# Kernel tuning notes

Hardware: AMD Instinct MI355X
Metric: run time of the kernel (lower is better)

The kernel has to match this reference:

```python
import jax, jax.numpy as jnp
import numpy as np

B, N, DIM, H, DH = 2, 1024, 1024, 8, 64
DI = H * DH  # 512
K = 4        # depthwise conv kernel
EPS = 1.1920929e-07  # float32 eps (torch RMSNorm default)


def setup_inputs() -> dict:
    key = jax.random.key(0)
    ks = jax.random.split(key, 12)
    s = lambda k, shape, sc=0.02: jax.random.normal(k, shape, jnp.float32) * sc
    return dict(
        x=jax.random.normal(ks[0], (B, N, DIM), jnp.float32),
        w_rms=jnp.ones((DIM,), jnp.float32),
        wq=s(ks[1], (DIM, DI)), wk=s(ks[2], (DIM, DI)), wv=s(ks[3], (DIM, DI)),
        wo=s(ks[4], (DI, DIM)),
        conv_q=s(ks[5], (DIM, K), 0.3), conv_k=s(ks[6], (DIM, K), 0.3), conv_v=s(ks[7], (DIM, K), 0.3),
        gamma_q=jnp.ones((H, 1, DH), jnp.float32), gamma_k=jnp.ones((H, 1, DH), jnp.float32),
        lr_w=s(ks[8], (DIM, H)), lr_b=jnp.full((H,), -4.0, jnp.float32),
        decay_w=s(ks[9], (DIM, H)), decay_b=jnp.full((H,), 4.0, jnp.float32),
        mom_w=s(ks[10], (DIM, H)), mom_b=jnp.full((H,), 2.0, jnp.float32),
    )


def rmsnorm(x, w):
    return x * jax.lax.rsqrt(jnp.mean(x * x, -1, keepdims=True) + EPS) * w


def mh_rmsnorm(x, gamma):  # x: (b, h, n, d)
    rms = jnp.sqrt(jnp.sum(x * x, -1, keepdims=True)) * (DH ** -0.5)
    return x / jnp.maximum(rms, 1e-8) * gamma


def dwconv(x, w):  # x: (b, n, dim), w: (dim, K) depthwise, padding K//2 -> length n+1
    y = jax.lax.conv_general_dilated(
        x.transpose(0, 2, 1), w[:, None, :], (1,), [(K // 2, K // 2)],
        feature_group_count=DIM, dimension_numbers=('NCW', 'OIW', 'NCW'))
    return y.transpose(0, 2, 1)


def gated_scan(a, x):  # h_t = a_t h_{t-1} + x_t, h_{-1}=0; a:(bh,t), x:(bh,t,d,d)
    def combine(c1, c2):
        a1, x1 = c1
        a2, x2 = c2
        return a1 * a2, a2 * x1 + x2
    _, h = jax.lax.associative_scan(combine, (a[..., None, None], x), axis=1)
    return h


def reference(x, w_rms, wq, wk, wv, wo, conv_q, conv_k, conv_v,
              gamma_q, gamma_k, lr_w, lr_b, decay_w, decay_b, mom_w, mom_b):
    b, n, _ = x.shape
    xa = rmsnorm(x, w_rms)
    qi, ki, vi = dwconv(xa, conv_q), dwconv(xa, conv_k), dwconv(xa, conv_v)
    split = lambda t: t.reshape(b, -1, H, DH).transpose(0, 2, 1, 3)[:, :, :n]  # (b,h,n,d)
    q = mh_rmsnorm(split(qi @ wq), gamma_q)
    k = mh_rmsnorm(split(ki @ wk), gamma_k)
    v = split(vi @ wv)
    fq = q.reshape(b * H, n, DH)
    fk = k.reshape(b * H, n, DH)
    fv = v.reshape(b * H, n, DH)
    sig = jax.nn.sigmoid
    lr = sig(xa @ lr_w + lr_b).transpose(0, 2, 1).reshape(b * H, n)
    decay = sig(xa @ decay_w + decay_b).transpose(0, 2, 1).reshape(b * H, n)
    mom = sig(xa @ mom_w + mom_b).transpose(0, 2, 1).reshape(b * H, n)
    # S_ref = S0 = 0 (fresh state) => pred = 0, delta_vec = -v
    g = jnp.einsum('bti,btj->btij', -fv, fk)          # (bh, n, d, d)
    Z = gated_scan(mom, g)                             # momentum scan
    S = gated_scan(decay, -lr[..., None, None] * Z)    # memory scan
    S_prev = jnp.concatenate([jnp.zeros_like(S[:, :1]), S[:, :-1]], axis=1)
    y = jnp.einsum('btdp,btp->btd', S_prev, fq)        # retrieval y_t = S_{t-1} psi_t
    y = y.reshape(b, H, n, DH).transpose(0, 2, 1, 3).reshape(b, n, DI)
    return y @ wo
```

## Files before the change

kernel.cpp:

```cpp
#include <hip/hip_runtime.h>
#include <math.h>

#define DEV __device__ __forceinline__

constexpr int Bb   = 2;
constexpr int Seq  = 1024;
constexpr int Dim  = 1024;
constexpr int Hh   = 8;
constexpr int Dh   = 64;
constexpr int Di   = 512;
constexpr int BN   = Bb * Seq;
constexpr int NSEQ = Bb * Hh;
constexpr int CHUNK = 32;
constexpr int CLEN  = Seq / CHUNK;
constexpr float EPSV = 1.1920929e-07f;
constexpr int NT   = 16;

typedef _Float16 half8 __attribute__((ext_vector_type(8)));
typedef float    f32x4 __attribute__((ext_vector_type(4)));

DEV float bf2f(unsigned short u) {
  union { unsigned int i; float f; } x; x.i = ((unsigned int)u) << 16; return x.f;
}
DEV unsigned short f2bf(float f) {
  union { float f; unsigned int i; } x; x.f = f;
  unsigned int r = x.i + 0x7fffu + ((x.i >> 16) & 1u);
  return (unsigned short)(r >> 16);
}
DEV float ldin(const void* p, int f32, size_t i) {
  if (f32) return ((const float*)p)[i];
  return bf2f(((const unsigned short*)p)[i]);
}

struct InPtrs { const void* p[17]; int n[17]; };

__global__ __launch_bounds__(64) void k_sniff(InPtrs ip, int* __restrict__ flags) {
  int b = blockIdx.x, tid = threadIdx.x;
  const unsigned short* u = (const unsigned short*)ip.p[b];
  int count = ip.n[b];
  int j = 2 * tid;
  int valid = 0, bad = 0;
  if (j < count) {
    valid = 1;
    float v = bf2f(u[j]);
    float a = fabsf(v);
    if (!(a >= 1e-12f && a <= 1e4f)) bad = 1;
  }
#pragma unroll
  for (int m = 1; m < 64; m <<= 1) { valid += __shfl_xor(valid, m); bad += __shfl_xor(bad, m); }
  if (tid == 0) flags[b] = (2 * bad > valid) ? 1 : 0;
}

__global__ __launch_bounds__(256) void k_prep_all(
    const void* __restrict__ wq, const void* __restrict__ wk,
    const void* __restrict__ wv, const void* __restrict__ wo,
    const void* __restrict__ lr_w, const void* __restrict__ decay_w,
    const void* __restrict__ mom_w,
    const void* __restrict__ cq, const void* __restrict__ ck,
    const void* __restrict__ cv,
    const void* __restrict__ gq, const void* __restrict__ gk,
    const void* __restrict__ lr_b, const void* __restrict__ decay_b,
    const void* __restrict__ mom_b,
    const int* __restrict__ flags,
    _Float16* __restrict__ wqT, _Float16* __restrict__ wkT,
    _Float16* __restrict__ wvT, _Float16* __restrict__ woT,
    _Float16* __restrict__ WgT,
    _Float16* __restrict__ wcq, _Float16* __restrict__ wck,
    _Float16* __restrict__ wcv,
    float* __restrict__ gqf, float* __restrict__ gkf, float* __restrict__ gbf)
{
  int blk = blockIdx.x;
  int tid = threadIdx.x;

  if (blk < 1024) {
    int z = blk >> 8, bx = blk & 15, by = (blk >> 4) & 15;
    const void* src = (z == 0) ? wq : ((z == 1) ? wk : ((z == 2) ? wv : wo));
    _Float16* dst   = (z == 0) ? wqT : ((z == 1) ? wkT : ((z == 2) ? wvT : woT));
    int f = flags[(z == 0) ? 2 : ((z == 1) ? 3 : ((z == 2) ? 4 : 5))];
    int Kd = (z < 3) ? Dim : Di;
    int Nn = (z < 3) ? Di : Dim;
    int n0 = bx * 64, k0 = by * 64;
    if (n0 >= Nn || k0 >= Kd) return;

    __shared__ float tile[64][65];
    int r = tid >> 4, c4 = (tid & 15) * 4;
#pragma unroll
    for (int rr = 0; rr < 4; ++rr) {
      int k = rr * 16 + r;
#pragma unroll
      for (int j = 0; j < 4; ++j)
        tile[k][c4 + j] = ldin(src, f, (size_t)(k0 + k) * Nn + n0 + c4 + j);
    }
    __syncthreads();
#pragma unroll
    for (int rr = 0; rr < 4; ++rr) {
      int n = rr * 16 + r;
      _Float16 o4[4];
#pragma unroll
      for (int j = 0; j < 4; ++j) o4[j] = (_Float16)tile[c4 + j][n];
      *(ushort4*)&dst[(size_t)(n0 + n) * Kd + k0 + c4] = *(ushort4*)o4;
    }
  } else if (blk < 1088) {
    int row = blk - 1024;
    if (row < 24) {
      int g = row >> 3, h = row & 7;
      const void* W = (g == 0) ? lr_w : ((g == 1) ? decay_w : mom_w);
      int f = (g == 0) ? flags[11] : ((g == 1) ? flags[13] : flags[15]);
#pragma unroll
      for (int it = 0; it < 4; ++it) {
        int d = it * 256 + tid;
        WgT[(size_t)row * Dim + d] = (_Float16)ldin(W, f, (size_t)d * Hh + h);
      }
    } else {
#pragma unroll
      for (int it = 0; it < 4; ++it)
        WgT[(size_t)row * Dim + it * 256 + tid] = (_Float16)0.f;
    }
  } else if (blk < 1104) {
    int e = (blk - 1088) * 256 + tid;
    int f6 = flags[6], f7 = flags[7], f8 = flags[8];
    wcq[e] = (_Float16)ldin(cq, f6, e);
    wck[e] = (_Float16)ldin(ck, f7, e);
    wcv[e] = (_Float16)ldin(cv, f8, e);
  } else {
    int f9 = flags[9], f10 = flags[10];
    for (int i = tid; i < Di; i += 256) {
      gqf[i] = ldin(gq, f9, i);
      gkf[i] = ldin(gk, f10, i);
    }
    if (tid < 24) {
      int g = tid >> 3, h = tid & 7;
      const void* Bp = (g == 0) ? lr_b : ((g == 1) ? decay_b : mom_b);
      int fB = (g == 0) ? flags[12] : ((g == 1) ? flags[14] : flags[16]);
      gbf[tid] = ldin(Bp, fB, h);
    }
  }
}

__global__ __launch_bounds__(256) void k_rms(
    const void* __restrict__ x, const void* __restrict__ w_rms,
    const int* __restrict__ flags, _Float16* __restrict__ xaf)
{
  __shared__ float red[4];
  int r = blockIdx.x;
  int tid = threadIdx.x, lane = tid & 63, wid = tid >> 6;
  int fx = flags[0], fw = flags[1];

  size_t rb = (size_t)r * Dim + tid * 4;
  float v0, v1, v2, v3;
  if (fx) {
    float4 u = *(const float4*)((const float*)x + rb);
    v0 = u.x; v1 = u.y; v2 = u.z; v3 = u.w;
  } else {
    ushort4 u = *(const ushort4*)((const unsigned short*)x + rb);
    v0 = bf2f(u.x); v1 = bf2f(u.y); v2 = bf2f(u.z); v3 = bf2f(u.w);
  }
  float ss = v0 * v0 + v1 * v1 + v2 * v2 + v3 * v3;
#pragma unroll
  for (int m = 1; m < 64; m <<= 1) ss += __shfl_xor(ss, m);
  if (lane == 0) red[wid] = ss;
  __syncthreads();
  float scale = rsqrtf((red[0] + red[1] + red[2] + red[3]) * (1.0f / Dim) + EPSV);

  float w0, w1, w2, w3;
  if (fw) {
    float4 u = *(const float4*)((const float*)w_rms + tid * 4);
    w0 = u.x; w1 = u.y; w2 = u.z; w3 = u.w;
  } else {
    ushort4 u = *(const ushort4*)((const unsigned short*)w_rms + tid * 4);
    w0 = bf2f(u.x); w1 = bf2f(u.y); w2 = bf2f(u.z); w3 = bf2f(u.w);
  }
  _Float16 t4[4] = {(_Float16)(v0 * scale * w0), (_Float16)(v1 * scale * w1),
                    (_Float16)(v2 * scale * w2), (_Float16)(v3 * scale * w3)};
  *(ushort4*)&xaf[rb] = *(ushort4*)t4;
}

__global__ __launch_bounds__(256) void k_gates(
    const _Float16* __restrict__ xaf, const _Float16* __restrict__ WgT,
    const float* __restrict__ gbf,
    float* __restrict__ lr, float* __restrict__ decay, float* __restrict__ mom)
{
  __shared__ __align__(16) _Float16 As[64][40];
  __shared__ __align__(16) _Float16 Bs[64][40];

  int tid = threadIdx.x, lane = tid & 63, wvid = tid >> 6;
  int m0 = blockIdx.x * 64;
  int srow = tid >> 2, scol = (tid & 3) * 8;
  int mrow = lane & 15, quad = lane >> 4;

  f32x4 acc[4];
#pragma unroll
  for (int mi = 0; mi < 4; ++mi) acc[mi] = (f32x4){0.f, 0.f, 0.f, 0.f};

  for (int kt = 0; kt < Dim; kt += 32) {
    __syncthreads();
    *(uint4*)&As[srow][scol] = *(const uint4*)&xaf[(size_t)(m0 + srow) * Dim + kt + scol];
    *(uint4*)&Bs[srow][scol] = *(const uint4*)&WgT[(size_t)srow * Dim + kt + scol];
    __syncthreads();
    half8 bfr = *(const half8*)&Bs[wvid * 16 + mrow][quad * 8];
#pragma unroll
    for (int mi = 0; mi < 4; ++mi) {
      half8 afr = *(const half8*)&As[mi * 16 + mrow][quad * 8];
      acc[mi] = __builtin_amdgcn_mfma_f32_16x16x32_f16(afr, bfr, acc[mi], 0, 0, 0);
    }
  }

  int col = wvid * 16 + mrow;
  if (col < 24) {
    int g = col >> 3, h = col & 7;
    float bias = gbf[col];
    float* Op = (g == 0) ? lr : ((g == 1) ? decay : mom);
#pragma unroll
    for (int mi = 0; mi < 4; ++mi) {
#pragma unroll
      for (int r2 = 0; r2 < 4; ++r2) {
        int row = m0 + mi * 16 + quad * 4 + r2;
        int b = row >> 10, t = row & (Seq - 1);
        float z = acc[mi][r2] + bias;
        Op[(b * Hh + h) * Seq + t] = 1.f / (1.f + expf(-z));
      }
    }
  }
}

__global__ __launch_bounds__(256) void k_conv(
    const _Float16* __restrict__ xaf,
    const _Float16* __restrict__ wcq, const _Float16* __restrict__ wck,
    const _Float16* __restrict__ wcv,
    _Float16* __restrict__ qc, _Float16* __restrict__ kc,
    _Float16* __restrict__ vc)
{
  int tb = blockIdx.x, b = blockIdx.y;
  int t0 = tb * NT;
  int c0 = threadIdx.x * 4;

  _Float16 lwq[16], lwk[16], lwv[16];
  *(uint4*)&lwq[0] = *(const uint4*)&wcq[c0 * 4];
  *(uint4*)&lwq[8] = *(const uint4*)&wcq[c0 * 4 + 8];
  *(uint4*)&lwk[0] = *(const uint4*)&wck[c0 * 4];
  *(uint4*)&lwk[8] = *(const uint4*)&wck[c0 * 4 + 8];
  *(uint4*)&lwv[0] = *(const uint4*)&wcv[c0 * 4];
  *(uint4*)&lwv[8] = *(const uint4*)&wcv[c0 * 4 + 8];

  float win[4][4];
  auto loadrow = [&](int ts, float dst[4]) {
    if (ts >= 0 && ts < Seq) {
      ushort4 u = *(const ushort4*)&xaf[((size_t)(b * Seq + ts)) * Dim + c0];
      _Float16 hx[4]; *(ushort4*)hx = u;
      dst[0] = (float)hx[0]; dst[1] = (float)hx[1];
      dst[2] = (float)hx[2]; dst[3] = (float)hx[3];
    } else {
      dst[0] = 0.f; dst[1] = 0.f; dst[2] = 0.f; dst[3] = 0.f;
    }
  };
  loadrow(t0 - 2, win[0]);
  loadrow(t0 - 1, win[1]);
  loadrow(t0,     win[2]);

#pragma unroll
  for (int tt = 0; tt < NT; ++tt) {
    int t = t0 + tt;
    loadrow(t + 1, win[(tt + 3) & 3]);
    const float* r0 = win[(tt + 0) & 3];
    const float* r1 = win[(tt + 1) & 3];
    const float* r2 = win[(tt + 2) & 3];
    const float* r3 = win[(tt + 3) & 3];

    _Float16 tq[4], tk[4], tv[4];
#pragma unroll
    for (int j = 0; j < 4; ++j) {
      float aq = r0[j] * (float)lwq[j * 4 + 0] + r1[j] * (float)lwq[j * 4 + 1]
               + r2[j] * (float)lwq[j * 4 + 2] + r3[j] * (float)lwq[j * 4 + 3];
      float ak = r0[j] * (float)lwk[j * 4 + 0] + r1[j] * (float)lwk[j * 4 + 1]
               + r2[j] * (float)lwk[j * 4 + 2] + r3[j] * (float)lwk[j * 4 + 3];
      float av = r0[j] * (float)lwv[j * 4 + 0] + r1[j] * (float)lwv[j * 4 + 1]
               + r2[j] * (float)lwv[j * 4 + 2] + r3[j] * (float)lwv[j * 4 + 3];
      tq[j] = (_Float16)aq; tk[j] = (_Float16)ak; tv[j] = (_Float16)av;
    }
    size_t o = ((size_t)(b * Seq + t)) * Dim + c0;
    *(ushort4*)&qc[o] = *(ushort4*)tq;
    *(ushort4*)&kc[o] = *(ushort4*)tk;
    *(ushort4*)&vc[o] = *(ushort4*)tv;
  }
}

__global__ __launch_bounds__(256) void k_gemm_128(
    const _Float16* __restrict__ A0, const _Float16* __restrict__ A1,
    const _Float16* __restrict__ A2,
    const _Float16* __restrict__ B0, const _Float16* __restrict__ B1,
    const _Float16* __restrict__ B2,
    void* __restrict__ C0, void* __restrict__ C1, void* __restrict__ C2,
    const int* __restrict__ flags,
    int Nn, int Kd, int is_final)
{
  int z = blockIdx.z;
  const _Float16* A  = (z == 0) ? A0 : ((z == 1) ? A1 : A2);
  const _Float16* Bt = (z == 0) ? B0 : ((z == 1) ? B1 : B2);
  void* C = (z == 0) ? C0 : ((z == 1) ? C1 : C2);

  __shared__ __align__(16) _Float16 As[128][40];
  __shared__ __align__(16) _Float16 Bs[64][40];

  int tid = threadIdx.x, lane = tid & 63, wv = tid >> 6;
  int n0 = blockIdx.x * 64, m0 = blockIdx.y * 128;
  int mrow = lane & 15, quad = lane >> 4;
  int wm = wv * 32;

  int ar0 = tid >> 2,        ac0 = (tid & 3) * 8;
  int ar1 = (tid + 256) >> 2;

  f32x4 acc[2][4];
#pragma unroll
  for (int mi = 0; mi < 2; ++mi)
#pragma unroll
    for (int ni = 0; ni < 4; ++ni) acc[mi][ni] = (f32x4){0.f, 0.f, 0.f, 0.f};

  for (int kt = 0; kt < Kd; kt += 32) {
    __syncthreads();
    *(uint4*)&As[ar0][ac0] = *(const uint4*)&A[(size_t)(m0 + ar0) * Kd + kt + ac0];
    *(uint4*)&As[ar1][ac0] = *(const uint4*)&A[(size_t)(m0 + ar1) * Kd + kt + ac0];
    *(uint4*)&Bs[ar0][ac0] = *(const uint4*)&Bt[(size_t)(n0 + ar0) * Kd + kt + ac0];
    __syncthreads();

    half8 bfr[4];
#pragma unroll
    for (int ni = 0; ni < 4; ++ni)
      bfr[ni] = *(const half8*)&Bs[ni * 16 + mrow][quad * 8];
#pragma unroll
    for (int mi = 0; mi < 2; ++mi) {
      half8 afr = *(const half8*)&As[wm + mi * 16 + mrow][quad * 8];
#pragma unroll
      for (int ni = 0; ni < 4; ++ni)
        acc[mi][ni] = __builtin_amdgcn_mfma_f32_16x16x32_f16(afr, bfr[ni], acc[mi][ni], 0, 0, 0);
    }
  }

  int any_bf16 = 0;
  if (is_final) {
#pragma unroll
    for (int i2 = 0; i2 < 17; ++i2) any_bf16 |= (flags[i2] == 0);
  }

#pragma unroll
  for (int mi = 0; mi < 2; ++mi) {
#pragma unroll
    for (int ni = 0; ni < 4; ++ni) {
      int col = n0 + ni * 16 + mrow;
#pragma unroll
      for (int r2 = 0; r2 < 4; ++r2) {
        int row = m0 + wm + mi * 16 + quad * 4 + r2;
        float v = acc[mi][ni][r2];
        size_t idx = (size_t)row * Nn + col;
        if (!is_final)        ((_Float16*)C)[idx] = (_Float16)v;
        else if (any_bf16)    ((unsigned short*)C)[idx] = f2bf(v);
        else                  ((float*)C)[idx] = v;
      }
    }
  }
}

__global__ __launch_bounds__(256) void k_phaseA(
    const _Float16* __restrict__ kpre, const _Float16* __restrict__ vpre,
    const float* __restrict__ gkf,
    const float* __restrict__ lr, const float* __restrict__ decay,
    const float* __restrict__ mom,
    _Float16* __restrict__ ZS_Z, _Float16* __restrict__ ZS_S,
    float* __restrict__ Mc, float* __restrict__ Dc, float* __restrict__ Wc)
{
  int c = blockIdx.x, s = blockIdx.y;
  int b = s >> 3, h = s & 7;
  int tid = threadIdx.x, lane = tid & 63, wv = tid >> 6;
  int i = tid >> 2, j0 = (tid & 3) * 16;
  __shared__ float kn[CLEN][64], vv[CLEN][64];
  __shared__ float gl[CLEN], gd[CLEN], gm[CLEN];

  {
    int t = tid >> 3, col = (tid & 7) * 8;
    size_t g = ((size_t)(b * Seq + c * CLEN + t)) * Di + h * 64 + col;
    half8 kv = *(const half8*)&kpre[g];
    half8 vvv = *(const half8*)&vpre[g];
#pragma unroll
    for (int j = 0; j < 8; ++j) { kn[t][col + j] = (float)kv[j]; vv[t][col + j] = (float)vvv[j]; }
    if (tid < 96) {
      int which = tid >> 5, t2 = tid & 31;
      const float* gp = (which == 0) ? lr : ((which == 1) ? decay : mom);
      float val = gp[s * Seq + c * CLEN + t2];
      if (which == 0) gl[t2] = val; else if (which == 1) gd[t2] = val; else gm[t2] = val;
    }
  }
  __syncthreads();
  {
    float gk = gkf[h * 64 + lane];
#pragma unroll
    for (int tt = 0; tt < 8; ++tt) {
      int t = wv * 8 + tt;
      float kvv = kn[t][lane];
      float ss = kvv * kvv;
#pragma unroll
      for (int m = 1; m < 64; m <<= 1) ss += __shfl_xor(ss, m);
      kn[t][lane] = kvv * (1.f / fmaxf(sqrtf(ss) * 0.125f, 1e-8f)) * gk;
    }
  }
  __syncthreads();

  float Zl[16], Sl[16];
#pragma unroll
  for (int jj = 0; jj < 16; ++jj) { Zl[jj] = 0.f; Sl[jj] = 0.f; }
  float Mcum = 1.f, Dcum = 1.f, wacc = 0.f;

  for (int t = 0; t < CLEN; ++t) {
    float l = gl[t], dd = gd[t], mm = gm[t];
    float vi = vv[t][i];
    Mcum *= mm;
#pragma unroll
    for (int jj = 0; jj < 16; ++jj) {
      Zl[jj] = fmaf(mm, Zl[jj], -vi * kn[t][j0 + jj]);
      Sl[jj] = fmaf(dd, Sl[jj], -l * Zl[jj]);
    }
    wacc = fmaf(dd, wacc, -l * Mcum);
    Dcum *= dd;
  }
  size_t base = ((size_t)(s * CHUNK + c)) * 4096 + (size_t)i * 64 + j0;
  half8 zo0, zo1, so0, so1;
#pragma unroll
  for (int jj = 0; jj < 8; ++jj) {
    zo0[jj] = (_Float16)Zl[jj];     zo1[jj] = (_Float16)Zl[jj + 8];
    so0[jj] = (_Float16)Sl[jj];     so1[jj] = (_Float16)Sl[jj + 8];
  }
  *(half8*)&ZS_Z[base] = zo0; *(half8*)&ZS_Z[base + 8] = zo1;
  *(half8*)&ZS_S[base] = so0; *(half8*)&ZS_S[base + 8] = so1;
  if (tid == 0) {
    Mc[s * CHUNK + c] = Mcum; Dc[s * CHUNK + c] = Dcum; Wc[s * CHUNK + c] = wacc;
  }
}

__global__ __launch_bounds__(256) void k_phaseB(
    _Float16* __restrict__ ZS_Z, _Float16* __restrict__ ZS_S,
    const float* __restrict__ Mc, const float* __restrict__ Dc,
    const float* __restrict__ Wc)
{
  int s = blockIdx.x;
  int e = blockIdx.y * 256 + threadIdx.x;
  float Z = 0.f, S = 0.f;
  for (int c = 0; c < CHUNK; ++c) {
    size_t base = ((size_t)(s * CHUNK + c)) * 4096 + e;
    float mc = Mc[s * CHUNK + c], dc = Dc[s * CHUNK + c], wc = Wc[s * CHUNK + c];
    float zl = (float)ZS_Z[base], sl = (float)ZS_S[base];
    ZS_Z[base] = (_Float16)Z; ZS_S[base] = (_Float16)S;
    S = fmaf(dc, S, fmaf(wc, Z, sl));
    Z = fmaf(mc, Z, zl);
  }
}

__global__ __launch_bounds__(256) void k_phaseC(
    const _Float16* __restrict__ qpre, const _Float16* __restrict__ kpre,
    const _Float16* __restrict__ vpre,
    const float* __restrict__ gqf, const float* __restrict__ gkf,
    const float* __restrict__ lr, const float* __restrict__ decay,
    const float* __restrict__ mom,
    const _Float16* __restrict__ ZS_Z, const _Float16* __restrict__ ZS_S,
    _Float16* __restrict__ yb)
{
  int c = blockIdx.x, s = blockIdx.y;
  int b = s >> 3, h = s & 7;
  int tid = threadIdx.x, lane = tid & 63, wv = tid >> 6;
  int i = tid >> 2, j0 = (tid & 3) * 16;
  __shared__ float kn[CLEN][64], vv[CLEN][64], qn[CLEN][64];
  __shared__ float gl[CLEN], gd[CLEN], gm[CLEN];

  float Zi_[16], Si_[16], Zl[16], Sl[16];
  size_t base = ((size_t)(s * CHUNK + c)) * 4096 + (size_t)i * 64 + j0;
  {
    half8 z0 = *(const half8*)&ZS_Z[base], z1 = *(const half8*)&ZS_Z[base + 8];
    half8 s0 = *(const half8*)&ZS_S[base], s1 = *(const half8*)&ZS_S[base + 8];
#pragma unroll
    for (int jj = 0; jj < 8; ++jj) {
      Zi_[jj] = (float)z0[jj]; Zi_[jj + 8] = (float)z1[jj];
      Si_[jj] = (float)s0[jj]; Si_[jj + 8] = (float)s1[jj];
      Zl[jj] = 0.f; Zl[jj + 8] = 0.f; Sl[jj] = 0.f; Sl[jj + 8] = 0.f;
    }
  }
  {
    int t = tid >> 3, col = (tid & 7) * 8;
    size_t g = ((size_t)(b * Seq + c * CLEN + t)) * Di + h * 64 + col;
    half8 kv = *(const half8*)&kpre[g];
    half8 vvv = *(const half8*)&vpre[g];
    half8 qv = *(const half8*)&qpre[g];
#pragma unroll
    for (int j = 0; j < 8; ++j) {
      kn[t][col + j] = (float)kv[j]; vv[t][col + j] = (float)vvv[j];
      qn[t][col + j] = (float)qv[j];
    }
    if (tid < 96) {
      int which = tid >> 5, t2 = tid & 31;
      const float* gp = (which == 0) ? lr : ((which == 1) ? decay : mom);
      float val = gp[s * Seq + c * CLEN + t2];
      if (which == 0) gl[t2] = val; else if (which == 1) gd[t2] = val; else gm[t2] = val;
    }
  }
  __syncthreads();
  {
    float gk = gkf[h * 64 + lane];
    float gq = gqf[h * 64 + lane];
#pragma unroll
    for (int tt = 0; tt < 8; ++tt) {
      int t = wv * 8 + tt;
      float kvv = kn[t][lane];
      float ssk = kvv * kvv;
      float qvv = qn[t][lane];
      float ssq = qvv * qvv;
#pragma unroll
      for (int m = 1; m < 64; m <<= 1) { ssk += __shfl_xor(ssk, m); ssq += __shfl_xor(ssq, m); }
      kn[t][lane] = kvv * (1.f / fmaxf(sqrtf(ssk) * 0.125f, 1e-8f)) * gk;
      qn[t][lane] = qvv * (1.f / fmaxf(sqrtf(ssq) * 0.125f, 1e-8f)) * gq;
    }
  }
  __syncthreads();

  float Mcum = 1.f, Dcum = 1.f, wacc = 0.f;
  float Dprev = 1.f, wprev = 0.f;

  for (int t = 0; t < CLEN; ++t) {
    float l = gl[t], dd = gd[t], mm = gm[t];

    float yp = 0.f;
#pragma unroll
    for (int jj = 0; jj < 16; ++jj) {
      float tmp = fmaf(Dprev, Si_[jj], fmaf(wprev, Zi_[jj], Sl[jj]));
      yp = fmaf(tmp, qn[t][j0 + jj], yp);
    }
    yp += __shfl_xor(yp, 1);
    yp += __shfl_xor(yp, 2);
    if ((tid & 3) == 0)
      yb[((size_t)(b * Seq + c * CLEN + t)) * Di + h * 64 + i] = (_Float16)yp;

    float vi = vv[t][i];
    Mcum *= mm;
#pragma unroll
    for (int jj = 0; jj < 16; ++jj) {
      Zl[jj] = fmaf(mm, Zl[jj], -vi * kn[t][j0 + jj]);
      Sl[jj] = fmaf(dd, Sl[jj], -l * Zl[jj]);
    }
    wacc = fmaf(dd, wacc, -l * Mcum);
    Dcum *= dd;
    Dprev = Dcum; wprev = wacc;
  }
}

extern "C" void kernel_launch(void* const* d_in, const int* in_sizes, int n_in,
                              void* d_out, int out_size, void* d_ws, size_t ws_size,
                              hipStream_t stream) {
  InPtrs ip;
  for (int i = 0; i < 17; ++i) { ip.p[i] = d_in[i]; ip.n[i] = in_sizes[i]; }

  char* p = (char*)d_ws;
  auto take = [&](size_t bytes) -> char* {
    char* q = p; p += (bytes + 255) & ~(size_t)255; return q;
  };
  int* flags           = (int*)take(32 * 4);
  _Float16* xaf        = (_Float16*)take((size_t)BN * Dim * 2);
  _Float16* qc         = (_Float16*)take((size_t)BN * Dim * 2);
  _Float16* kc         = (_Float16*)take((size_t)BN * Dim * 2);
  _Float16* vc         = (_Float16*)take((size_t)BN * Dim * 2);
  _Float16* qpre       = (_Float16*)take((size_t)BN * Di * 2);
  _Float16* kpre       = (_Float16*)take((size_t)BN * Di * 2);
  _Float16* vpre       = (_Float16*)take((size_t)BN * Di * 2);
  float* lrA           = (float*)take((size_t)NSEQ * Seq * 4);
  float* decayA        = (float*)take((size_t)NSEQ * Seq * 4);
  float* momA          = (float*)take((size_t)NSEQ * Seq * 4);
  float* Mc            = (float*)take((size_t)NSEQ * CHUNK * 4);
  float* Dc            = (float*)take((size_t)NSEQ * CHUNK * 4);
  float* Wc            = (float*)take((size_t)NSEQ * CHUNK * 4);
  _Float16* wqT        = (_Float16*)take((size_t)Di * Dim * 2);
  _Float16* wkT        = (_Float16*)take((size_t)Di * Dim * 2);
  _Float16* wvT        = (_Float16*)take((size_t)Di * Dim * 2);
  _Float16* woT        = (_Float16*)take((size_t)Dim * Di * 2);
  _Float16* WgT        = (_Float16*)take((size_t)64 * Dim * 2);
  _Float16* wcq        = (_Float16*)take((size_t)Dim * 4 * 2);
  _Float16* wck        = (_Float16*)take((size_t)Dim * 4 * 2);
  _Float16* wcv        = (_Float16*)take((size_t)Dim * 4 * 2);
  float* gqf           = (float*)take(Di * 4);
  float* gkf           = (float*)take(Di * 4);
  float* gbf           = (float*)take(32 * 4);
  _Float16* ZS_Z       = qc;
  _Float16* ZS_S       = kc;
  _Float16* yb         = vc;

  k_sniff<<<17, 64, 0, stream>>>(ip, flags);
  k_prep_all<<<1105, 256, 0, stream>>>(
      d_in[2], d_in[3], d_in[4], d_in[5],
      d_in[11], d_in[13], d_in[15],
      d_in[6], d_in[7], d_in[8],
      d_in[9], d_in[10], d_in[12], d_in[14], d_in[16],
      flags, wqT, wkT, wvT, woT, WgT, wcq, wck, wcv, gqf, gkf, gbf);

  k_rms<<<BN, 256, 0, stream>>>(d_in[0], d_in[1], flags, xaf);
  k_gates<<<BN / 64, 256, 0, stream>>>(xaf, WgT, gbf, lrA, decayA, momA);
  k_conv<<<dim3(Seq / NT, Bb), 256, 0, stream>>>(xaf, wcq, wck, wcv, qc, kc, vc);

  dim3 g1(Di / 64, BN / 128, 3);
  k_gemm_128<<<g1, 256, 0, stream>>>(qc, kc, vc, wqT, wkT, wvT,
                                     qpre, kpre, vpre, flags, Di, Dim, 0);

  k_phaseA<<<dim3(CHUNK, NSEQ), 256, 0, stream>>>(kpre, vpre, gkf,
                                                  lrA, decayA, momA,
                                                  ZS_Z, ZS_S, Mc, Dc, Wc);
  k_phaseB<<<dim3(NSEQ, 16), 256, 0, stream>>>(ZS_Z, ZS_S, Mc, Dc, Wc);
  k_phaseC<<<dim3(CHUNK, NSEQ), 256, 0, stream>>>(qpre, kpre, vpre, gqf, gkf,
                                                  lrA, decayA, momA,
                                                  ZS_Z, ZS_S, yb);

  dim3 g2(Dim / 64, BN / 128, 1);
  k_gemm_128<<<g2, 256, 0, stream>>>(yb, yb, yb, woT, woT, woT,
                                     d_out, d_out, d_out, flags, Dim, Di, 1);
}
```

Baseline: 208.4 us.

## Fuse RMSNorm with depthwise conv, split-K gate GEMM, fold sniff into prep

Merges the dtype-sniff kernel into the weight-prep kernel, so each prep block recomputes its own input format flag. Fuses RMSNorm into the depthwise conv kernel, normalizing rows with halo into shared memory and writing xaf once. Splits the gate GEMM over K into eight partial slabs, and moves the reduction, bias and sigmoid into the scan phase kernels. The aim is fewer launches and more parallelism in the small gate GEMM, at the cost of redundant halo normalization, redundant sniffing per prep block, and extra partial-sum reads in phaseA and phaseC.

Result: faster. 195.6 us (-6.1%).

```diff
diff --git a/kernel.cpp b/kernel.cpp
--- a/kernel.cpp
+++ b/kernel.cpp
@@ -14,7 +14,8 @@
 constexpr int CHUNK = 32;
 constexpr int CLEN  = Seq / CHUNK;
 constexpr float EPSV = 1.1920929e-07f;
-constexpr int NT   = 16;
+constexpr int NT2  = 8;
+constexpr int KSPL = 8;
 
 typedef _Float16 half8 __attribute__((ext_vector_type(8)));
 typedef float    f32x4 __attribute__((ext_vector_type(4)));
@@ -31,37 +32,24 @@
   if (f32) return ((const float*)p)[i];
   return bf2f(((const unsigned short*)p)[i]);
 }
-
-struct InPtrs { const void* p[17]; int n[17]; };
-
-__global__ __launch_bounds__(64) void k_sniff(InPtrs ip, int* __restrict__ flags) {
-  int b = blockIdx.x, tid = threadIdx.x;
-  const unsigned short* u = (const unsigned short*)ip.p[b];
-  int count = ip.n[b];
-  int j = 2 * tid;
-  int valid = 0, bad = 0;
-  if (j < count) {
+DEV int sniff_vote(const void* p, int n, int tid) {
+  int j = 2 * tid, valid = 0, bad = 0;
+  if (j < n) {
     valid = 1;
-    float v = bf2f(u[j]);
+    float v = bf2f(((const unsigned short*)p)[j]);
     float a = fabsf(v);
     if (!(a >= 1e-12f && a <= 1e4f)) bad = 1;
   }
 #pragma unroll
   for (int m = 1; m < 64; m <<= 1) { valid += __shfl_xor(valid, m); bad += __shfl_xor(bad, m); }
-  if (tid == 0) flags[b] = (2 * bad > valid) ? 1 : 0;
-}
+  return (2 * bad > valid) ? 1 : 0;
+}
+
+struct InPtrs { const void* p[17]; int n[17]; };
 
 __global__ __launch_bounds__(256) void k_prep_all(
-    const void* __restrict__ wq, const void* __restrict__ wk,
-    const void* __restrict__ wv, const void* __restrict__ wo,
-    const void* __restrict__ lr_w, const void* __restrict__ decay_w,
-    const void* __restrict__ mom_w,
-    const void* __restrict__ cq, const void* __restrict__ ck,
-    const void* __restrict__ cv,
-    const void* __restrict__ gq, const void* __restrict__ gk,
-    const void* __restrict__ lr_b, const void* __restrict__ decay_b,
-    const void* __restrict__ mom_b,
-    const int* __restrict__ flags,
+    InPtrs ip,
+    int* __restrict__ flags,
     _Float16* __restrict__ wqT, _Float16* __restrict__ wkT,
     _Float16* __restrict__ wvT, _Float16* __restrict__ woT,
     _Float16* __restrict__ WgT,
@@ -71,17 +59,22 @@
 {
   int blk = blockIdx.x;
   int tid = threadIdx.x;
+  __shared__ int sfl[8];
 
   if (blk < 1024) {
     int z = blk >> 8, bx = blk & 15, by = (blk >> 4) & 15;
-    const void* src = (z == 0) ? wq : ((z == 1) ? wk : ((z == 2) ? wv : wo));
+    int idx = (z == 0) ? 2 : ((z == 1) ? 3 : ((z == 2) ? 4 : 5));
+    const void* src = ip.p[idx];
     _Float16* dst   = (z == 0) ? wqT : ((z == 1) ? wkT : ((z == 2) ? wvT : woT));
-    int f = flags[(z == 0) ? 2 : ((z == 1) ? 3 : ((z == 2) ? 4 : 5))];
     int Kd = (z < 3) ? Dim : Di;
     int Nn = (z < 3) ? Di : Dim;
     int n0 = bx * 64, k0 = by * 64;
     if (n0 >= Nn || k0 >= Kd) return;
 
+    if (tid < 64) { int f = sniff_vote(src, ip.n[idx], tid); if (tid == 0) sfl[0] = f; }
+    __syncthreads();
+    int f = sfl[0];
+
     __shared__ float tile[64][65];
     int r = tid >> 4, c4 = (tid & 15) * 4;
 #pragma unroll
@@ -104,8 +97,11 @@
     int row = blk - 1024;
     if (row < 24) {
       int g = row >> 3, h = row & 7;
-      const void* W = (g == 0) ? lr_w : ((g == 1) ? decay_w : mom_w);
-      int f = (g == 0) ? flags[11] : ((g == 1) ? flags[13] : flags[15]);
+      int idx = (g == 0) ? 11 : ((g == 1) ? 13 : 15);
+      const void* W = ip.p[idx];
+      if (tid < 64) { int f = sniff_vote(W, ip.n[idx], tid); if (tid == 0) sfl[0] = f; }
+      __syncthreads();
+      int f = sfl[0];
 #pragma unroll
       for (int it = 0; it < 4; ++it) {
         int d = it * 256 + tid;
@@ -117,122 +113,94 @@
         WgT[(size_t)row * Dim + it * 256 + tid] = (_Float16)0.f;
     }
   } else if (blk < 1104) {
+    if (tid < 64) {
+      int f6 = sniff_vote(ip.p[6], ip.n[6], tid);
+      int f7 = sniff_vote(ip.p[7], ip.n[7], tid);
+      int f8 = sniff_vote(ip.p[8], ip.n[8], tid);
+      if (tid == 0) { sfl[0] = f6; sfl[1] = f7; sfl[2] = f8; }
+    }
+    __syncthreads();
     int e = (blk - 1088) * 256 + tid;
-    int f6 = flags[6], f7 = flags[7], f8 = flags[8];
-    wcq[e] = (_Float16)ldin(cq, f6, e);
-    wck[e] = (_Float16)ldin(ck, f7, e);
-    wcv[e] = (_Float16)ldin(cv, f8, e);
+    wcq[e] = (_Float16)ldin(ip.p[6], sfl[0], e);
+    wck[e] = (_Float16)ldin(ip.p[7], sfl[1], e);
+    wcv[e] = (_Float16)ldin(ip.p[8], sfl[2], e);
   } else {
-    int f9 = flags[9], f10 = flags[10];
+    __shared__ int allf[17];
+    for (int ii = 0; ii < 17; ++ii) {
+      if (tid < 64) {
+        int f = sniff_vote(ip.p[ii], ip.n[ii], tid);
+        if (tid == 0) { flags[ii] = f; allf[ii] = f; }
+      }
+    }
+    __syncthreads();
+    int f9 = allf[9], f10 = allf[10];
     for (int i = tid; i < Di; i += 256) {
-      gqf[i] = ldin(gq, f9, i);
-      gkf[i] = ldin(gk, f10, i);
+      gqf[i] = ldin(ip.p[9], f9, i);
+      gkf[i] = ldin(ip.p[10], f10, i);
     }
     if (tid < 24) {
       int g = tid >> 3, h = tid & 7;
-      const void* Bp = (g == 0) ? lr_b : ((g == 1) ? decay_b : mom_b);
-      int fB = (g == 0) ? flags[12] : ((g == 1) ? flags[14] : flags[16]);
-      gbf[tid] = ldin(Bp, fB, h);
-    }
-  }
-}
-
-__global__ __launch_bounds__(256) void k_rms(
+      int idx = (g == 0) ? 12 : ((g == 1) ? 14 : 16);
+      gbf[tid] = ldin(ip.p[idx], allf[idx], h);
+    }
+  }
+}
+
+__global__ __launch_bounds__(256) void k_rmsconv(
     const void* __restrict__ x, const void* __restrict__ w_rms,
-    const int* __restrict__ flags, _Float16* __restrict__ xaf)
-{
+    const int* __restrict__ flags,
+    const _Float16* __restrict__ wcq, const _Float16* __restrict__ wck,
+    const _Float16* __restrict__ wcv,
+    _Float16* __restrict__ xaf,
+    _Float16* __restrict__ qc, _Float16* __restrict__ kc,
+    _Float16* __restrict__ vc)
+{
+  constexpr int NR = NT2 + 3;
+  __shared__ _Float16 xas[NR][Dim];
   __shared__ float red[4];
-  int r = blockIdx.x;
+  int tb = blockIdx.x, b = blockIdx.y;
+  int t0 = tb * NT2;
   int tid = threadIdx.x, lane = tid & 63, wid = tid >> 6;
+  int c0 = tid * 4;
   int fx = flags[0], fw = flags[1];
-
-  size_t rb = (size_t)r * Dim + tid * 4;
-  float v0, v1, v2, v3;
-  if (fx) {
-    float4 u = *(const float4*)((const float*)x + rb);
-    v0 = u.x; v1 = u.y; v2 = u.z; v3 = u.w;
-  } else {
-    ushort4 u = *(const ushort4*)((const unsigned short*)x + rb);
-    v0 = bf2f(u.x); v1 = bf2f(u.y); v2 = bf2f(u.z); v3 = bf2f(u.w);
-  }
-  float ss = v0 * v0 + v1 * v1 + v2 * v2 + v3 * v3;
-#pragma unroll
-  for (int m = 1; m < 64; m <<= 1) ss += __shfl_xor(ss, m);
-  if (lane == 0) red[wid] = ss;
-  __syncthreads();
-  float scale = rsqrtf((red[0] + red[1] + red[2] + red[3]) * (1.0f / Dim) + EPSV);
 
   float w0, w1, w2, w3;
   if (fw) {
-    float4 u = *(const float4*)((const float*)w_rms + tid * 4);
+    float4 u = *(const float4*)((const float*)w_rms + c0);
     w0 = u.x; w1 = u.y; w2 = u.z; w3 = u.w;
   } else {
-    ushort4 u = *(const ushort4*)((const unsigned short*)w_rms + tid * 4);
+    ushort4 u = *(const ushort4*)((const unsigned short*)w_rms + c0);
     w0 = bf2f(u.x); w1 = bf2f(u.y); w2 = bf2f(u.z); w3 = bf2f(u.w);
   }
-  _Float16 t4[4] = {(_Float16)(v0 * scale * w0), (_Float16)(v1 * scale * w1),
-                    (_Float16)(v2 * scale * w2), (_Float16)(v3 * scale * w3)};
-  *(ushort4*)&xaf[rb] = *(ushort4*)t4;
-}
-
-__global__ __launch_bounds__(256) void k_gates(
-    const _Float16* __restrict__ xaf, const _Float16* __restrict__ WgT,
-    const float* __restrict__ gbf,
-    float* __restrict__ lr, float* __restrict__ decay, float* __restrict__ mom)
-{
-  __shared__ __align__(16) _Float16 As[64][40];
-  __shared__ __align__(16) _Float16 Bs[64][40];
-
-  int tid = threadIdx.x, lane = tid & 63, wvid = tid >> 6;
-  int m0 = blockIdx.x * 64;
-  int srow = tid >> 2, scol = (tid & 3) * 8;
-  int mrow = lane & 15, quad = lane >> 4;
-
-  f32x4 acc[4];
-#pragma unroll
-  for (int mi = 0; mi < 4; ++mi) acc[mi] = (f32x4){0.f, 0.f, 0.f, 0.f};
-
-  for (int kt = 0; kt < Dim; kt += 32) {
-    __syncthreads();
-    *(uint4*)&As[srow][scol] = *(const uint4*)&xaf[(size_t)(m0 + srow) * Dim + kt + scol];
-    *(uint4*)&Bs[srow][scol] = *(const uint4*)&WgT[(size_t)srow * Dim + kt + scol];
-    __syncthreads();
-    half8 bfr = *(const half8*)&Bs[wvid * 16 + mrow][quad * 8];
-#pragma unroll
-    for (int mi = 0; mi < 4; ++mi) {
-      half8 afr = *(const half8*)&As[mi * 16 + mrow][quad * 8];
-      acc[mi] = __builtin_amdgcn_mfma_f32_16x16x32_f16(afr, bfr, acc[mi], 0, 0, 0);
-    }
-  }
-
-  int col = wvid * 16 + mrow;
-  if (col < 24) {
-    int g = col >> 3, h = col & 7;
-    float bias = gbf[col];
-    float* Op = (g == 0) ? lr : ((g == 1) ? decay : mom);
-#pragma unroll
-    for (int mi = 0; mi < 4; ++mi) {
-#pragma unroll
-      for (int r2 = 0; r2 < 4; ++r2) {
-        int row = m0 + mi * 16 + quad * 4 + r2;
-        int b = row >> 10, t = row & (Seq - 1);
-        float z = acc[mi][r2] + bias;
-        Op[(b * Hh + h) * Seq + t] = 1.f / (1.f + expf(-z));
+
+  for (int rr = 0; rr < NR; ++rr) {
+    int r = t0 - 2 + rr;
+    float v0 = 0.f, v1 = 0.f, v2 = 0.f, v3 = 0.f;
+    bool inr = (r >= 0 && r < Seq);
+    if (inr) {
+      size_t rb = (size_t)(b * Seq + r) * Dim + c0;
+      if (fx) {
+        float4 u = *(const float4*)((const float*)x + rb);
+        v0 = u.x; v1 = u.y; v2 = u.z; v3 = u.w;
+      } else {
+        ushort4 u = *(const ushort4*)((const unsigned short*)x + rb);
+        v0 = bf2f(u.x); v1 = bf2f(u.y); v2 = bf2f(u.z); v3 = bf2f(u.w);
       }
     }
-  }
-}
-
-__global__ __launch_bounds__(256) void k_conv(
-    const _Float16* __restrict__ xaf,
-    const _Float16* __restrict__ wcq, const _Float16* __restrict__ wck,
-    const _Float16* __restrict__ wcv,
-    _Float16* __restrict__ qc, _Float16* __restrict__ kc,
-    _Float16* __restrict__ vc)
-{
-  int tb = blockIdx.x, b = blockIdx.y;
-  int t0 = tb * NT;
-  int c0 = threadIdx.x * 4;
+    float ss = v0 * v0 + v1 * v1 + v2 * v2 + v3 * v3;
+#pragma unroll
+    for (int m = 1; m < 64; m <<= 1) ss += __shfl_xor(ss, m);
+    if (lane == 0) red[wid] = ss;
+    __syncthreads();
+    float scale = rsqrtf((red[0] + red[1] + red[2] + red[3]) * (1.0f / Dim) + EPSV);
+
+    _Float16 t4[4] = {(_Float16)(v0 * scale * w0), (_Float16)(v1 * scale * w1),
+                      (_Float16)(v2 * scale * w2), (_Float16)(v3 * scale * w3)};
+    *(ushort4*)&xas[rr][c0] = *(ushort4*)t4;
+    if (inr && r >= t0 && r < t0 + NT2)
+      *(ushort4*)&xaf[(size_t)(b * Seq + r) * Dim + c0] = *(ushort4*)t4;
+    __syncthreads();
+  }
 
   _Float16 lwq[16], lwk[16], lwv[16];
   *(uint4*)&lwq[0] = *(const uint4*)&wcq[c0 * 4];
@@ -242,45 +210,74 @@
   *(uint4*)&lwv[0] = *(const uint4*)&wcv[c0 * 4];
   *(uint4*)&lwv[8] = *(const uint4*)&wcv[c0 * 4 + 8];
 
-  float win[4][4];
-  auto loadrow = [&](int ts, float dst[4]) {
-    if (ts >= 0 && ts < Seq) {
-      ushort4 u = *(const ushort4*)&xaf[((size_t)(b * Seq + ts)) * Dim + c0];
-      _Float16 hx[4]; *(ushort4*)hx = u;
-      dst[0] = (float)hx[0]; dst[1] = (float)hx[1];
-      dst[2] = (float)hx[2]; dst[3] = (float)hx[3];
-    } else {
-      dst[0] = 0.f; dst[1] = 0.f; dst[2] = 0.f; dst[3] = 0.f;
-    }
-  };
-  loadrow(t0 - 2, win[0]);
-  loadrow(t0 - 1, win[1]);
-  loadrow(t0,     win[2]);
-
-#pragma unroll
-  for (int tt = 0; tt < NT; ++tt) {
-    int t = t0 + tt;
-    loadrow(t + 1, win[(tt + 3) & 3]);
-    const float* r0 = win[(tt + 0) & 3];
-    const float* r1 = win[(tt + 1) & 3];
-    const float* r2 = win[(tt + 2) & 3];
-    const float* r3 = win[(tt + 3) & 3];
-
+#pragma unroll
+  for (int tt = 0; tt < NT2; ++tt) {
+    float rv[4][4];
+#pragma unroll
+    for (int k = 0; k < 4; ++k) {
+      _Float16 hx[4];
+      *(ushort4*)hx = *(const ushort4*)&xas[tt + k][c0];
+#pragma unroll
+      for (int j = 0; j < 4; ++j) rv[k][j] = (float)hx[j];
+    }
     _Float16 tq[4], tk[4], tv[4];
 #pragma unroll
     for (int j = 0; j < 4; ++j) {
-      float aq = r0[j] * (float)lwq[j * 4 + 0] + r1[j] * (float)lwq[j * 4 + 1]
-               + r2[j] * (float)lwq[j * 4 + 2] + r3[j] * (float)lwq[j * 4 + 3];
-      float ak = r0[j] * (float)lwk[j * 4 + 0] + r1[j] * (float)lwk[j * 4 + 1]
-               + r2[j] * (float)lwk[j * 4 + 2] + r3[j] * (float)lwk[j * 4 + 3];
-      float av = r0[j] * (float)lwv[j * 4 + 0] + r1[j] * (float)lwv[j * 4 + 1]
-               + r2[j] * (float)lwv[j * 4 + 2] + r3[j] * (float)lwv[j * 4 + 3];
+      float aq = rv[0][j] * (float)lwq[j * 4 + 0] + rv[1][j] * (float)lwq[j * 4 + 1]
+               + rv[2][j] * (float)lwq[j * 4 + 2] + rv[3][j] * (float)lwq[j * 4 + 3];
+      float ak = rv[0][j] * (float)lwk[j * 4 + 0] + rv[1][j] * (float)lwk[j * 4 + 1]
+               + rv[2][j] * (float)lwk[j * 4 + 2] + rv[3][j] * (float)lwk[j * 4 + 3];
+      float av = rv[0][j] * (float)lwv[j * 4 + 0] + rv[1][j] * (float)lwv[j * 4 + 1]
+               + rv[2][j] * (float)lwv[j * 4 + 2] + rv[3][j] * (float)lwv[j * 4 + 3];
       tq[j] = (_Float16)aq; tk[j] = (_Float16)ak; tv[j] = (_Float16)av;
     }
-    size_t o = ((size_t)(b * Seq + t)) * Dim + c0;
+    size_t o = ((size_t)(b * Seq + t0 + tt)) * Dim + c0;
     *(ushort4*)&qc[o] = *(ushort4*)tq;
     *(ushort4*)&kc[o] = *(ushort4*)tk;
     *(ushort4*)&vc[o] = *(ushort4*)tv;
+  }
+}
+
+__global__ __launch_bounds__(256) void k_gates(
+    const _Float16* __restrict__ xaf, const _Float16* __restrict__ WgT,
+    float* __restrict__ gpart)
+{
+  __shared__ __align__(16) _Float16 As[64][40];
+  __shared__ __align__(16) _Float16 Bs[64][40];
+
+  int tid = threadIdx.x, lane = tid & 63, wvid = tid >> 6;
+  int m0 = blockIdx.x * 64, ks = blockIdx.y;
+  int srow = tid >> 2, scol = (tid & 3) * 8;
+  int mrow = lane & 15, quad = lane >> 4;
+  int kbase = ks * (Dim / KSPL);
+
+  f32x4 acc[4];
+#pragma unroll
+  for (int mi = 0; mi < 4; ++mi) acc[mi] = (f32x4){0.f, 0.f, 0.f, 0.f};
+
+  for (int kt = kbase; kt < kbase + Dim / KSPL; kt += 32) {
+    __syncthreads();
+    *(uint4*)&As[srow][scol] = *(const uint4*)&xaf[(size_t)(m0 + srow) * Dim + kt + scol];
+    *(uint4*)&Bs[srow][scol] = *(const uint4*)&WgT[(size_t)srow * Dim + kt + scol];
+    __syncthreads();
+    half8 bfr = *(const half8*)&Bs[wvid * 16 + mrow][quad * 8];
+#pragma unroll
+    for (int mi = 0; mi < 4; ++mi) {
+      half8 afr = *(const half8*)&As[mi * 16 + mrow][quad * 8];
+      acc[mi] = __builtin_amdgcn_mfma_f32_16x16x32_f16(afr, bfr, acc[mi], 0, 0, 0);
+    }
+  }
+
+  int col = wvid * 16 + mrow;
+  if (col < 24) {
+#pragma unroll
+    for (int mi = 0; mi < 4; ++mi) {
+#pragma unroll
+      for (int r2 = 0; r2 < 4; ++r2) {
+        int row = m0 + mi * 16 + quad * 4 + r2;
+        gpart[((size_t)ks * BN + row) * 32 + col] = acc[mi][r2];
+      }
+    }
   }
 }
 
@@ -306,7 +303,7 @@
   int mrow = lane & 15, quad = lane >> 4;
   int wm = wv * 32;
 
-  int ar0 = tid >> 2,        ac0 = (tid & 3) * 8;
+  int ar0 = tid >> 2, ac0 = (tid & 3) * 8;
   int ar1 = (tid + 256) >> 2;
 
   f32x4 acc[2][4];
@@ -359,11 +356,27 @@
   }
 }
 
+DEV void load_gates(const float* __restrict__ gpart, const float* __restrict__ gbf,
+                    int b, int h, int c, int tid,
+                    float* gl, float* gd, float* gm)
+{
+  if (tid < 96) {
+    int which = tid >> 5, t2 = tid & 31;
+    int col = which * 8 + h;
+    int row = b * Seq + c * CLEN + t2;
+    float acc = gbf[col];
+#pragma unroll
+    for (int ks = 0; ks < KSPL; ++ks)
+      acc += gpart[((size_t)ks * BN + row) * 32 + col];
+    float sg = 1.f / (1.f + expf(-acc));
+    if (which == 0) gl[t2] = sg; else if (which == 1) gd[t2] = sg; else gm[t2] = sg;
+  }
+}
+
 __global__ __launch_bounds__(256) void k_phaseA(
     const _Float16* __restrict__ kpre, const _Float16* __restrict__ vpre,
     const float* __restrict__ gkf,
-    const float* __restrict__ lr, const float* __restrict__ decay,
-    const float* __restrict__ mom,
+    const float* __restrict__ gpart, const float* __restrict__ gbf,
     _Float16* __restrict__ ZS_Z, _Float16* __restrict__ ZS_S,
     float* __restrict__ Mc, float* __restrict__ Dc, float* __restrict__ Wc)
 {
@@ -381,12 +394,7 @@
     half8 vvv = *(const half8*)&vpre[g];
 #pragma unroll
     for (int j = 0; j < 8; ++j) { kn[t][col + j] = (float)kv[j]; vv[t][col + j] = (float)vvv[j]; }
-    if (tid < 96) {
-      int which = tid >> 5, t2 = tid & 31;
-      const float* gp = (which == 0) ? lr : ((which == 1) ? decay : mom);
-      float val = gp[s * Seq + c * CLEN + t2];
-      if (which == 0) gl[t2] = val; else if (which == 1) gd[t2] = val; else gm[t2] = val;
-    }
+    load_gates(gpart, gbf, b, h, c, tid, gl, gd, gm);
   }
   __syncthreads();
   {
@@ -456,8 +464,7 @@
     const _Float16* __restrict__ qpre, const _Float16* __restrict__ kpre,
     const _Float16* __restrict__ vpre,
     const float* __restrict__ gqf, const float* __restrict__ gkf,
-    const float* __restrict__ lr, const float* __restrict__ decay,
-    const float* __restrict__ mom,
+    const float* __restrict__ gpart, const float* __restrict__ gbf,
     const _Float16* __restrict__ ZS_Z, const _Float16* __restrict__ ZS_S,
     _Float16* __restrict__ yb)
 {
@@ -491,12 +498,7 @@
       kn[t][col + j] = (float)kv[j]; vv[t][col + j] = (float)vvv[j];
       qn[t][col + j] = (float)qv[j];
     }
-    if (tid < 96) {
-      int which = tid >> 5, t2 = tid & 31;
-      const float* gp = (which == 0) ? lr : ((which == 1) ? decay : mom);
-      float val = gp[s * Seq + c * CLEN + t2];
-      if (which == 0) gl[t2] = val; else if (which == 1) gd[t2] = val; else gm[t2] = val;
-    }
+    load_gates(gpart, gbf, b, h, c, tid, gl, gd, gm);
   }
   __syncthreads();
   {
@@ -565,9 +567,7 @@
   _Float16* qpre       = (_Float16*)take((size_t)BN * Di * 2);
   _Float16* kpre       = (_Float16*)take((size_t)BN * Di * 2);
   _Float16* vpre       = (_Float16*)take((size_t)BN * Di * 2);
-  float* lrA           = (float*)take((size_t)NSEQ * Seq * 4);
-  float* decayA        = (float*)take((size_t)NSEQ * Seq * 4);
-  float* momA          = (float*)take((size_t)NSEQ * Seq * 4);
+  float* gpart         = (float*)take((size_t)KSPL * BN * 32 * 4);
   float* Mc            = (float*)take((size_t)NSEQ * CHUNK * 4);
   float* Dc            = (float*)take((size_t)NSEQ * CHUNK * 4);
   float* Wc            = (float*)take((size_t)NSEQ * CHUNK * 4);
@@ -586,28 +586,24 @@
   _Float16* ZS_S       = kc;
   _Float16* yb         = vc;
 
-  k_sniff<<<17, 64, 0, stream>>>(ip, flags);
-  k_prep_all<<<1105, 256, 0, stream>>>(
-      d_in[2], d_in[3], d_in[4], d_in[5],
-      d_in[11], d_in[13], d_in[15],
-      d_in[6], d_in[7], d_in[8],
-      d_in[9], d_in[10], d_in[12], d_in[14], d_in[16],
-      flags, wqT, wkT, wvT, woT, WgT, wcq, wck, wcv, gqf, gkf, gbf);
-
-  k_rms<<<BN, 256, 0, stream>>>(d_in[0], d_in[1], flags, xaf);
-  k_gates<<<BN / 64, 256, 0, stream>>>(xaf, WgT, gbf, lrA, decayA, momA);
-  k_conv<<<dim3(Seq / NT, Bb), 256, 0, stream>>>(xaf, wcq, wck, wcv, qc, kc, vc);
+  k_prep_all<<<1105, 256, 0, stream>>>(ip, flags, wqT, wkT, wvT, woT, WgT,
+                                       wcq, wck, wcv, gqf, gkf, gbf);
+
+  k_rmsconv<<<dim3(Seq / NT2, Bb), 256, 0, stream>>>(
+      d_in[0], d_in[1], flags, wcq, wck, wcv, xaf, qc, kc, vc);
+
+  k_gates<<<dim3(BN / 64, KSPL), 256, 0, stream>>>(xaf, WgT, gpart);
 
   dim3 g1(Di / 64, BN / 128, 3);
   k_gemm_128<<<g1, 256, 0, stream>>>(qc, kc, vc, wqT, wkT, wvT,
                                      qpre, kpre, vpre, flags, Di, Dim, 0);
 
   k_phaseA<<<dim3(CHUNK, NSEQ), 256, 0, stream>>>(kpre, vpre, gkf,
-                                                  lrA, decayA, momA,
+                                                  gpart, gbf,
                                                   ZS_Z, ZS_S, Mc, Dc, Wc);
   k_phaseB<<<dim3(NSEQ, 16), 256, 0, stream>>>(ZS_Z, ZS_S, Mc, Dc, Wc);
   k_phaseC<<<dim3(CHUNK, NSEQ), 256, 0, stream>>>(qpre, kpre, vpre, gqf, gkf,
-                                                  lrA, decayA, momA,
+                                                  gpart, gbf,
                                                   ZS_Z, ZS_S, yb);
 
   dim3 g2(Dim / 64, BN / 128, 1);
```
